# Performance work log

Measured on AMD Instinct MI355X. Metric: run time of the kernel, lower is better.

## Reference

```python
import jax, jax.numpy as jnp
import numpy as np

N_NODES = 100000
N_EDGES = 1600000
D_IN = 128
D_HID = 128
N_CLASSES = 64


def _sage_mean_layer(h, src, dst, deg, W_self, W_neigh, b):
    # gather source-node features along edges: [E, d]
    msg = h[src]
    # sum messages into destination nodes, then mean by in-degree
    agg = jax.ops.segment_sum(msg, dst, num_segments=N_NODES)
    mean_neigh = agg / deg[:, None]
    return jax.nn.relu(h @ W_self + mean_neigh @ W_neigh + b)


def setup_inputs() -> dict:
    key = jax.random.key(0)
    ks = jax.random.split(key, 9)
    s = 1.0 / np.sqrt(D_IN)
    return {
        "features": jax.random.normal(ks[0], (N_NODES, D_IN), dtype=jnp.float32),
        "src": jax.random.randint(ks[1], (N_EDGES,), 0, N_NODES, dtype=jnp.int32),
        "dst": jax.random.randint(ks[2], (N_EDGES,), 0, N_NODES, dtype=jnp.int32),
        "W_self1": jax.random.normal(ks[3], (D_IN, D_HID), dtype=jnp.float32) * s,
        "W_neigh1": jax.random.normal(ks[4], (D_IN, D_HID), dtype=jnp.float32) * s,
        "b1": jnp.zeros((D_HID,), dtype=jnp.float32),
        "W_self2": jax.random.normal(ks[5], (D_HID, D_HID), dtype=jnp.float32) * s,
        "W_neigh2": jax.random.normal(ks[6], (D_HID, D_HID), dtype=jnp.float32) * s,
        "b2": jnp.zeros((D_HID,), dtype=jnp.float32),
        "W_out": jax.random.normal(ks[7], (D_HID, N_CLASSES), dtype=jnp.float32) * s,
        "b_out": jnp.zeros((N_CLASSES,), dtype=jnp.float32),
    }


def reference(features, src, dst, W_self1, W_neigh1, b1, W_self2, W_neigh2, b2, W_out, b_out):
    # in-degree per destination node (clamped to avoid div-by-zero for isolated nodes)
    deg = jax.ops.segment_sum(jnp.ones((N_EDGES,), jnp.float32), dst, num_segments=N_NODES)
    deg = jnp.maximum(deg, 1.0)
    h = _sage_mean_layer(features, src, dst, deg, W_self1, W_neigh1, b1)
    h = _sage_mean_layer(h, src, dst, deg, W_self2, W_neigh2, b2)
    return h @ W_out + b_out  # [N_NODES, N_CLASSES] logits
```

## Files before the change

### kernel.cpp

```cpp
#include <hip/hip_runtime.h>
#include <hip/hip_bf16.h>

constexpr int N_NODES = 100000;
constexpr int N_EDGES = 1600000;
constexpr int D = 128;
constexpr int N_CLASSES = 64;

constexpr int PART_NODES = 32;
constexpr int NPART = N_NODES / PART_NODES;
constexpr int NB1 = 49;
constexpr int CAP1 = 40960;
constexpr int SUBB = 10;
constexpr int CHUNK = CAP1 / SUBB;
constexpr int CAP2 = 1024;
constexpr int NCTR2 = NB1 * 64;
constexpr int EB1 = (N_EDGES + 1023) / 1024;
constexpr int CIB = 13;
constexpr int CVTB = N_NODES * (D / 4) / 256;
constexpr int PKB = 36;

typedef __attribute__((ext_vector_type(8))) short short8;
typedef __attribute__((ext_vector_type(4))) float f32x4;
typedef __attribute__((ext_vector_type(2))) float f32x2;

static __device__ __forceinline__ float bf2f(unsigned int lo16) {
    unsigned int x = lo16 << 16;
    return __builtin_bit_cast(float, x);
}
static __device__ __forceinline__ unsigned short f2bf(float f) {
    unsigned int x = __builtin_bit_cast(unsigned int, f);
    x += 0x7fffu + ((x >> 16) & 1u);
    return (unsigned short)(x >> 16);
}
static __device__ __forceinline__ unsigned int pack4_fp8(float a, float b,
                                                         float c, float d) {
    int v = __builtin_amdgcn_cvt_pk_fp8_f32(a, b, 0, false);
    v = __builtin_amdgcn_cvt_pk_fp8_f32(c, d, v, true);
    return (unsigned int)v;
}
static __device__ __forceinline__ unsigned char f2fp8(float a) {
    return (unsigned char)(__builtin_amdgcn_cvt_pk_fp8_f32(a, a, 0, false) & 0xff);
}

__global__ __launch_bounds__(256) void prep_k(int* __restrict__ cursor1,
                                              int* __restrict__ cursor2,
                                              const float* __restrict__ feat,
                                              unsigned short* __restrict__ fbuf,
                                              unsigned int* __restrict__ f8buf,
                                              const float* __restrict__ Ws1,
                                              const float* __restrict__ Wn1,
                                              const float* __restrict__ Ws2,
                                              const float* __restrict__ Wn2,
                                              const float* __restrict__ Wo,
                                              unsigned short* __restrict__ wp1,
                                              unsigned short* __restrict__ wp2,
                                              unsigned short* __restrict__ wpo) {
    const int b = blockIdx.x;
    const int t = threadIdx.x;
    if (b < CIB) {
        int i = b * 256 + t;
        if (i < NB1) cursor1[i] = i * CAP1;
        if (i < NCTR2) cursor2[i] = i << 10;
    } else if (b < CIB + CVTB) {
        int i = (b - CIB) * 256 + t;
        float4 v = ((const float4*)feat)[i];
        ushort4 r;
        r.x = f2bf(v.x); r.y = f2bf(v.y); r.z = f2bf(v.z); r.w = f2bf(v.w);
        ((ushort4*)fbuf)[i] = r;
        f8buf[i] = pack4_fp8(v.x, v.y, v.z, v.w);
    } else {
        int g = (b - CIB - CVTB) * 4 + (t >> 6);
        if (g >= 144) return;
        int lane = t & 63;
        const float *Wa, *Wb;
        unsigned short* wp;
        int DOUT, bb;
        if (g < 64)       { Wa = Ws1; Wb = Wn1; wp = wp1; DOUT = 128; bb = g; }
        else if (g < 128) { Wa = Ws2; Wb = Wn2; wp = wp2; DOUT = 128; bb = g - 64; }
        else              { Wa = Wo;  Wb = nullptr; wp = wpo; DOUT = 64; bb = g - 128; }
        int NCT = DOUT / 16;
        int kstep = bb / NCT;
        int ct = bb % NCT;
        int col = ct * 16 + (lane & 15);
        int kbase = kstep * 32 + (lane >> 4) * 8;
        unsigned short r[8];
        #pragma unroll
        for (int j = 0; j < 8; ++j) {
            int k = kbase + j;
            float w = (k < 128) ? Wa[(size_t)k * DOUT + col]
                                : Wb[(size_t)(k - 128) * DOUT + col];
            r[j] = f2bf(w);
        }
        *(short8*)(wp + ((size_t)((kstep * NCT + ct) * 64 + lane)) * 8) =
            *(const short8*)r;
    }
}

__global__ __launch_bounds__(256) void bin1_k(const int* __restrict__ src,
                                              const int* __restrict__ dst,
                                              int* __restrict__ cursor1,
                                              unsigned int* __restrict__ pack1) {
    __shared__ unsigned int lpay[1024];
    __shared__ unsigned char lcb[1024];
    __shared__ int hist[NB1], loff[NB1], gpos[NB1], lcur[NB1];

    const int t = threadIdx.x;
    const int ebase = blockIdx.x * 1024;
    int nblk = N_EDGES - ebase;
    if (nblk > 1024) nblk = 1024;
    const bool ok = (t * 4 < nblk);

    if (t < NB1) hist[t] = 0;
    __syncthreads();

    int4 d4, s4;
    if (ok) {
        d4 = *(const int4*)(dst + ebase + t * 4);
        s4 = *(const int4*)(src + ebase + t * 4);
        atomicAdd(&hist[d4.x >> 11], 1);
        atomicAdd(&hist[d4.y >> 11], 1);
        atomicAdd(&hist[d4.z >> 11], 1);
        atomicAdd(&hist[d4.w >> 11], 1);
    }
    __syncthreads();

    if (t == 0) {
        int run = 0;
        #pragma unroll
        for (int b = 0; b < NB1; ++b) { loff[b] = run; run += hist[b]; }
    }
    __syncthreads();
    if (t < NB1) {
        gpos[t] = atomicAdd(cursor1 + t, hist[t]);
        lcur[t] = loff[t];
    }
    __syncthreads();

    if (ok) {
        #pragma unroll
        for (int k = 0; k < 4; ++k) {
            int dd = (k == 0) ? d4.x : (k == 1) ? d4.y : (k == 2) ? d4.z : d4.w;
            int ss = (k == 0) ? s4.x : (k == 1) ? s4.y : (k == 2) ? s4.z : s4.w;
            int cb = dd >> 11;
            int pos = atomicAdd(&lcur[cb], 1);
            lpay[pos] = ((unsigned int)(dd & 2047) << 17) | (unsigned int)ss;
            lcb[pos] = (unsigned char)cb;
        }
    }
    __syncthreads();

    for (int i = t; i < nblk; i += 256) {
        int cb = lcb[i];
        int op = gpos[cb] + (i - loff[cb]);
        if (op < (cb + 1) * CAP1) pack1[op] = lpay[i];
    }
}

__global__ __launch_bounds__(256) void bin2_k(const int* __restrict__ cursor1,
                                              int* __restrict__ cursor2,
                                              const unsigned int* __restrict__ pack1,
                                              unsigned int* __restrict__ pack2) {
    __shared__ unsigned int lpay[CHUNK];
    __shared__ unsigned int lsort[CHUNK];
    __shared__ int hist[64], loff[64], gpos[64], lcur[64];

    const int t = threadIdx.x;
    const int cb = blockIdx.x / SUBB;
    const int sb = blockIdx.x % SUBB;

    int cnt = cursor1[cb] - cb * CAP1;
    if (cnt > CAP1) cnt = CAP1;
    const int base = sb * CHUNK;
    int n = cnt - base;
    if (n <= 0) return;
    if (n > CHUNK) n = CHUNK;

    if (t < 64) hist[t] = 0;
    __syncthreads();

    const unsigned int* gsrc = pack1 + (size_t)cb * CAP1 + base;
    for (int i = t; i < n; i += 256) {
        unsigned int pk = gsrc[i];
        lpay[i] = pk;
        atomicAdd(&hist[pk >> 22], 1);
    }
    __syncthreads();

    if (t == 0) {
        int run = 0;
        #pragma unroll
        for (int b = 0; b < 64; ++b) { loff[b] = run; run += hist[b]; }
    }
    __syncthreads();
    if (t < 64) {
        gpos[t] = atomicAdd(cursor2 + cb * 64 + t, hist[t]);
        lcur[t] = loff[t];
    }
    __syncthreads();

    for (int i = t; i < n; i += 256) {
        unsigned int pk = lpay[i];
        int pos = atomicAdd(&lcur[pk >> 22], 1);
        lsort[pos] = pk;
    }
    __syncthreads();

    for (int i = t; i < n; i += 256) {
        unsigned int pk = lsort[i];
        int pw = pk >> 22;
        int p = cb * 64 + pw;
        int op = gpos[pw] + (i - loff[pw]);
        if (op < ((p + 1) << 10)) pack2[op] = pk & 0x003fffffu;
    }
}

template <bool OUTPROJ>
__global__ __launch_bounds__(256) void fused_k(const unsigned short* __restrict__ xin,
                                               const unsigned char* __restrict__ x8,
                                               const unsigned int* __restrict__ pack,
                                               const int* __restrict__ cursor2,
                                               const short8* __restrict__ wp,
                                               const float* __restrict__ bias,
                                               unsigned short* __restrict__ xout,
                                               unsigned char* __restrict__ x8out,
                                               const short8* __restrict__ wpo,
                                               const float* __restrict__ bout,
                                               float* __restrict__ outp) {
    __shared__ unsigned int eraw[CAP2];
    __shared__ unsigned int ssrc[CAP2];
    __shared__ int nsh;
    __shared__ int bcnt[32];
    __shared__ int boff[33];
    __shared__ unsigned short mlds[PART_NODES][136];

    const int t = threadIdx.x;
    const int p = blockIdx.x;

    if (t == 0) {
        int c = cursor2[p] - (p << 10);
        nsh = (c < CAP2) ? c : CAP2;
    }
    if (t < 32) bcnt[t] = 0;
    __syncthreads();
    const int n = nsh;

    const unsigned int* gsrc = pack + ((size_t)p << 10);
    for (int i = t; i < n; i += 256) {
        unsigned int pk = gsrc[i];
        eraw[i] = pk;
        atomicAdd(&bcnt[pk >> 17], 1);
    }
    __syncthreads();

    if (t == 0) {
        int s = 0;
        #pragma unroll
        for (int i = 0; i < 32; ++i) { boff[i] = s; s += bcnt[i]; }
        boff[32] = s;
    }
    __syncthreads();
    if (t < 32) bcnt[t] = boff[t];
    __syncthreads();

    for (int i = t; i < n; i += 256) {
        unsigned int pk = eraw[i];
        int pos = atomicAdd(&bcnt[pk >> 17], 1);
        ssrc[pos] = pk & 0x1ffffu;
    }
    __syncthreads();

    const int w = t >> 6, lane = t & 63;
    const int sub = lane >> 4;
    const int cl = lane & 15;

    for (int g = 0; g < 8; ++g) {
        const int ni = w * 8 + g;
        const int b = boff[ni];
        const int eN = boff[ni + 1];

        float acc[8];
        #pragma unroll
        for (int r = 0; r < 8; ++r) acc[r] = 0.f;

        int i = b + sub;
        for (; i + 4 < eN; i += 8) {
            int s0 = ssrc[i];
            int s1 = ssrc[i + 4];
            uint2 u0 = *(const uint2*)(x8 + (size_t)s0 * 128 + cl * 8);
            uint2 u1 = *(const uint2*)(x8 + (size_t)s1 * 128 + cl * 8);
            f32x2 q;
            q = __builtin_amdgcn_cvt_pk_f32_fp8(u0.x, false); acc[0] += q[0]; acc[1] += q[1];
            q = __builtin_amdgcn_cvt_pk_f32_fp8(u0.x, true);  acc[2] += q[0]; acc[3] += q[1];
            q = __builtin_amdgcn_cvt_pk_f32_fp8(u0.y, false); acc[4] += q[0]; acc[5] += q[1];
            q = __builtin_amdgcn_cvt_pk_f32_fp8(u0.y, true);  acc[6] += q[0]; acc[7] += q[1];
            q = __builtin_amdgcn_cvt_pk_f32_fp8(u1.x, false); acc[0] += q[0]; acc[1] += q[1];
            q = __builtin_amdgcn_cvt_pk_f32_fp8(u1.x, true);  acc[2] += q[0]; acc[3] += q[1];
            q = __builtin_amdgcn_cvt_pk_f32_fp8(u1.y, false); acc[4] += q[0]; acc[5] += q[1];
            q = __builtin_amdgcn_cvt_pk_f32_fp8(u1.y, true);  acc[6] += q[0]; acc[7] += q[1];
        }
        if (i < eN) {
            int s0 = ssrc[i];
            uint2 u0 = *(const uint2*)(x8 + (size_t)s0 * 128 + cl * 8);
            f32x2 q;
            q = __builtin_amdgcn_cvt_pk_f32_fp8(u0.x, false); acc[0] += q[0]; acc[1] += q[1];
            q = __builtin_amdgcn_cvt_pk_f32_fp8(u0.x, true);  acc[2] += q[0]; acc[3] += q[1];
            q = __builtin_amdgcn_cvt_pk_f32_fp8(u0.y, false); acc[4] += q[0]; acc[5] += q[1];
            q = __builtin_amdgcn_cvt_pk_f32_fp8(u0.y, true);  acc[6] += q[0]; acc[7] += q[1];
        }
        #pragma unroll
        for (int r = 0; r < 8; ++r) {
            acc[r] += __shfl_xor(acc[r], 16);
            acc[r] += __shfl_xor(acc[r], 32);
        }
        float inv = 1.0f / fmaxf((float)(eN - b), 1.0f);
        float lo = acc[sub * 2 + 0] * inv;
        float hi = acc[sub * 2 + 1] * inv;
        unsigned int o = ((unsigned int)f2bf(hi) << 16) | (unsigned int)f2bf(lo);
        *(unsigned int*)(&mlds[ni][cl * 8 + sub * 2]) = o;
    }
    __syncthreads();

    const int frag = w & 1;
    const int cg0 = (w >> 1) * 4;
    const int r15 = lane & 15;
    const int khi = lane >> 4;
    const int row0 = p * PART_NODES + frag * 16;
    const unsigned short* arow = xin + (size_t)(row0 + r15) * 128 + khi * 8;

    f32x4 acc[4];
    #pragma unroll
    for (int c = 0; c < 4; ++c) acc[c] = {0.f, 0.f, 0.f, 0.f};

    #pragma unroll
    for (int ks = 0; ks < 8; ++ks) {
        short8 a;
        if (ks < 4) a = *(const short8*)(arow + ks * 32);
        else        a = *(const short8*)(&mlds[frag * 16 + r15][(ks - 4) * 32 + khi * 8]);
        #pragma unroll
        for (int c = 0; c < 4; ++c) {
            short8 b = wp[(ks * 8 + cg0 + c) * 64 + lane];
            acc[c] = __builtin_amdgcn_mfma_f32_16x16x32_bf16(a, b, acc[c], 0, 0, 0);
        }
    }

    const int rhi = khi, col0 = r15;
    if (!OUTPROJ) {
        #pragma unroll
        for (int c = 0; c < 4; ++c) {
            float bv = bias[(cg0 + c) * 16 + col0];
            #pragma unroll
            for (int j = 0; j < 4; ++j) {
                float v = fmaxf(acc[c][j] + bv, 0.f);
                size_t off = (size_t)(row0 + rhi * 4 + j) * 128 + (cg0 + c) * 16 + col0;
                xout[off] = f2bf(v);
                x8out[off] = f2fp8(v);
            }
        }
    } else {
        __syncthreads();
        #pragma unroll
        for (int c = 0; c < 4; ++c) {
            float bv = bias[(cg0 + c) * 16 + col0];
            #pragma unroll
            for (int j = 0; j < 4; ++j) {
                float v = fmaxf(acc[c][j] + bv, 0.f);
                mlds[frag * 16 + rhi * 4 + j][(cg0 + c) * 16 + col0] = f2bf(v);
            }
        }
        __syncthreads();
        const int frag2 = w & 1;
        const int ct0 = (w >> 1) * 2;
        f32x4 oacc[2];
        oacc[0] = {0.f, 0.f, 0.f, 0.f};
        oacc[1] = {0.f, 0.f, 0.f, 0.f};
        #pragma unroll
        for (int ks = 0; ks < 4; ++ks) {
            short8 a = *(const short8*)(&mlds[frag2 * 16 + r15][ks * 32 + khi * 8]);
            #pragma unroll
            for (int c = 0; c < 2; ++c) {
                short8 b = wpo[(ks * 4 + ct0 + c) * 64 + lane];
                oacc[c] = __builtin_amdgcn_mfma_f32_16x16x32_bf16(a, b, oacc[c], 0, 0, 0);
            }
        }
        #pragma unroll
        for (int c = 0; c < 2; ++c) {
            float bv = bout[(ct0 + c) * 16 + col0];
            #pragma unroll
            for (int j = 0; j < 4; ++j) {
                outp[(size_t)(p * PART_NODES + frag2 * 16 + rhi * 4 + j) * N_CLASSES
                     + (ct0 + c) * 16 + col0] = oacc[c][j] + bv;
            }
        }
    }
}

extern "C" void kernel_launch(void* const* d_in, const int* in_sizes, int n_in,
                              void* d_out, int out_size, void* d_ws, size_t ws_size,
                              hipStream_t stream) {
    const float* feat   = (const float*)d_in[0];
    const int*   src    = (const int*)d_in[1];
    const int*   dst    = (const int*)d_in[2];
    const float* Wself1 = (const float*)d_in[3];
    const float* Wneigh1= (const float*)d_in[4];
    const float* b1     = (const float*)d_in[5];
    const float* Wself2 = (const float*)d_in[6];
    const float* Wneigh2= (const float*)d_in[7];
    const float* b2     = (const float*)d_in[8];
    const float* Wout   = (const float*)d_in[9];
    const float* bout   = (const float*)d_in[10];
    float* out = (float*)d_out;
    (void)ws_size;

    int* cursor1 = (int*)d_ws;
    int* cursor2 = cursor1 + 64;
    unsigned int* pack1 = (unsigned int*)(cursor2 + NCTR2);
    unsigned int* pack2 = pack1 + (size_t)NB1 * CAP1;
    unsigned short* fbuf1 = (unsigned short*)(pack2 + (size_t)NCTR2 * CAP2);
    unsigned short* h1    = fbuf1 + (size_t)N_NODES * D;
    unsigned int* f8feat  = (unsigned int*)(h1 + (size_t)N_NODES * D);
    unsigned int* h1f8    = f8feat + (size_t)N_NODES * (D / 4);
    unsigned short* wp1   = (unsigned short*)(h1f8 + (size_t)N_NODES * (D / 4));
    unsigned short* wp2   = wp1 + 256 * 128;
    unsigned short* wpo   = wp2 + 256 * 128;

    prep_k<<<CIB + CVTB + PKB, 256, 0, stream>>>(cursor1, cursor2, feat,
                                                 fbuf1, f8feat,
                                                 Wself1, Wneigh1, Wself2, Wneigh2,
                                                 Wout, wp1, wp2, wpo);

    bin1_k<<<EB1, 256, 0, stream>>>(src, dst, cursor1, pack1);
    bin2_k<<<NB1 * SUBB, 256, 0, stream>>>(cursor1, cursor2, pack1, pack2);

    fused_k<false><<<NPART, 256, 0, stream>>>(fbuf1, (const unsigned char*)f8feat,
                                              pack2, cursor2,
                                              (const short8*)wp1, b1, h1,
                                              (unsigned char*)h1f8,
                                              nullptr, nullptr, nullptr);

    fused_k<true><<<NPART, 256, 0, stream>>>(h1, (const unsigned char*)h1f8,
                                             pack2, cursor2,
                                             (const short8*)wp2, b2, nullptr, nullptr,
                                             (const short8*)wpo, bout, out);
}
```

Measured before the change: 177.9 us.

## Merge edge binning into prep kernel, memset cursors, unroll gather by four

```diff
diff --git a/kernel.cpp b/kernel.cpp
--- a/kernel.cpp
+++ b/kernel.cpp
@@ -15,7 +15,6 @@
 constexpr int CAP2 = 1024;
 constexpr int NCTR2 = NB1 * 64;
 constexpr int EB1 = (N_EDGES + 1023) / 1024;
-constexpr int CIB = 13;
 constexpr int CVTB = N_NODES * (D / 4) / 256;
 constexpr int PKB = 36;
 
@@ -41,9 +40,18 @@
 static __device__ __forceinline__ unsigned char f2fp8(float a) {
     return (unsigned char)(__builtin_amdgcn_cvt_pk_fp8_f32(a, a, 0, false) & 0xff);
 }
-
-__global__ __launch_bounds__(256) void prep_k(int* __restrict__ cursor1,
-                                              int* __restrict__ cursor2,
+static __device__ __forceinline__ void dec8(uint2 u, float* acc) {
+    f32x2 q;
+    q = __builtin_amdgcn_cvt_pk_f32_fp8(u.x, false); acc[0] += q[0]; acc[1] += q[1];
+    q = __builtin_amdgcn_cvt_pk_f32_fp8(u.x, true);  acc[2] += q[0]; acc[3] += q[1];
+    q = __builtin_amdgcn_cvt_pk_f32_fp8(u.y, false); acc[4] += q[0]; acc[5] += q[1];
+    q = __builtin_amdgcn_cvt_pk_f32_fp8(u.y, true);  acc[6] += q[0]; acc[7] += q[1];
+}
+
+__global__ __launch_bounds__(256) void prep_k(const int* __restrict__ src,
+                                              const int* __restrict__ dst,
+                                              int* __restrict__ cursor1,
+                                              unsigned int* __restrict__ pack1,
                                               const float* __restrict__ feat,
                                               unsigned short* __restrict__ fbuf,
                                               unsigned int* __restrict__ f8buf,
@@ -55,21 +63,72 @@
                                               unsigned short* __restrict__ wp1,
                                               unsigned short* __restrict__ wp2,
                                               unsigned short* __restrict__ wpo) {
+    __shared__ unsigned int lpay[1024];
+    __shared__ unsigned char lcb[1024];
+    __shared__ int hist[NB1], loff[NB1], gpos[NB1], lcur[NB1];
+
     const int b = blockIdx.x;
     const int t = threadIdx.x;
-    if (b < CIB) {
-        int i = b * 256 + t;
-        if (i < NB1) cursor1[i] = i * CAP1;
-        if (i < NCTR2) cursor2[i] = i << 10;
-    } else if (b < CIB + CVTB) {
-        int i = (b - CIB) * 256 + t;
+
+    if (b < EB1) {
+        const int ebase = b * 1024;
+        int nblk = N_EDGES - ebase;
+        if (nblk > 1024) nblk = 1024;
+        const bool ok = (t * 4 < nblk);
+
+        if (t < NB1) hist[t] = 0;
+        __syncthreads();
+
+        int4 d4, s4;
+        if (ok) {
+            d4 = *(const int4*)(dst + ebase + t * 4);
+            s4 = *(const int4*)(src + ebase + t * 4);
+            atomicAdd(&hist[d4.x >> 11], 1);
+            atomicAdd(&hist[d4.y >> 11], 1);
+            atomicAdd(&hist[d4.z >> 11], 1);
+            atomicAdd(&hist[d4.w >> 11], 1);
+        }
+        __syncthreads();
+
+        if (t == 0) {
+            int run = 0;
+            #pragma unroll
+            for (int k = 0; k < NB1; ++k) { loff[k] = run; run += hist[k]; }
+        }
+        __syncthreads();
+        if (t < NB1) {
+            gpos[t] = atomicAdd(cursor1 + t, hist[t]);
+            lcur[t] = loff[t];
+        }
+        __syncthreads();
+
+        if (ok) {
+            #pragma unroll
+            for (int k = 0; k < 4; ++k) {
+                int dd = (k == 0) ? d4.x : (k == 1) ? d4.y : (k == 2) ? d4.z : d4.w;
+                int ss = (k == 0) ? s4.x : (k == 1) ? s4.y : (k == 2) ? s4.z : s4.w;
+                int cb = dd >> 11;
+                int pos = atomicAdd(&lcur[cb], 1);
+                lpay[pos] = ((unsigned int)(dd & 2047) << 17) | (unsigned int)ss;
+                lcb[pos] = (unsigned char)cb;
+            }
+        }
+        __syncthreads();
+
+        for (int i = t; i < nblk; i += 256) {
+            int cb = lcb[i];
+            int rel = gpos[cb] + (i - loff[cb]);
+            if (rel < CAP1) pack1[(size_t)cb * CAP1 + rel] = lpay[i];
+        }
+    } else if (b < EB1 + CVTB) {
+        int i = (b - EB1) * 256 + t;
         float4 v = ((const float4*)feat)[i];
         ushort4 r;
         r.x = f2bf(v.x); r.y = f2bf(v.y); r.z = f2bf(v.z); r.w = f2bf(v.w);
         ((ushort4*)fbuf)[i] = r;
         f8buf[i] = pack4_fp8(v.x, v.y, v.z, v.w);
     } else {
-        int g = (b - CIB - CVTB) * 4 + (t >> 6);
+        int g = (b - EB1 - CVTB) * 4 + (t >> 6);
         if (g >= 144) return;
         int lane = t & 63;
         const float *Wa, *Wb;
@@ -96,66 +155,6 @@
     }
 }
 
-__global__ __launch_bounds__(256) void bin1_k(const int* __restrict__ src,
-                                              const int* __restrict__ dst,
-                                              int* __restrict__ cursor1,
-                                              unsigned int* __restrict__ pack1) {
-    __shared__ unsigned int lpay[1024];
-    __shared__ unsigned char lcb[1024];
-    __shared__ int hist[NB1], loff[NB1], gpos[NB1], lcur[NB1];
-
-    const int t = threadIdx.x;
-    const int ebase = blockIdx.x * 1024;
-    int nblk = N_EDGES - ebase;
-    if (nblk > 1024) nblk = 1024;
-    const bool ok = (t * 4 < nblk);
-
-    if (t < NB1) hist[t] = 0;
-    __syncthreads();
-
-    int4 d4, s4;
-    if (ok) {
-        d4 = *(const int4*)(dst + ebase + t * 4);
-        s4 = *(const int4*)(src + ebase + t * 4);
-        atomicAdd(&hist[d4.x >> 11], 1);
-        atomicAdd(&hist[d4.y >> 11], 1);
-        atomicAdd(&hist[d4.z >> 11], 1);
-        atomicAdd(&hist[d4.w >> 11], 1);
-    }
-    __syncthreads();
-
-    if (t == 0) {
-        int run = 0;
-        #pragma unroll
-        for (int b = 0; b < NB1; ++b) { loff[b] = run; run += hist[b]; }
-    }
-    __syncthreads();
-    if (t < NB1) {
-        gpos[t] = atomicAdd(cursor1 + t, hist[t]);
-        lcur[t] = loff[t];
-    }
-    __syncthreads();
-
-    if (ok) {
-        #pragma unroll
-        for (int k = 0; k < 4; ++k) {
-            int dd = (k == 0) ? d4.x : (k == 1) ? d4.y : (k == 2) ? d4.z : d4.w;
-            int ss = (k == 0) ? s4.x : (k == 1) ? s4.y : (k == 2) ? s4.z : s4.w;
-            int cb = dd >> 11;
-            int pos = atomicAdd(&lcur[cb], 1);
-            lpay[pos] = ((unsigned int)(dd & 2047) << 17) | (unsigned int)ss;
-            lcb[pos] = (unsigned char)cb;
-        }
-    }
-    __syncthreads();
-
-    for (int i = t; i < nblk; i += 256) {
-        int cb = lcb[i];
-        int op = gpos[cb] + (i - loff[cb]);
-        if (op < (cb + 1) * CAP1) pack1[op] = lpay[i];
-    }
-}
-
 __global__ __launch_bounds__(256) void bin2_k(const int* __restrict__ cursor1,
                                               int* __restrict__ cursor2,
                                               const unsigned int* __restrict__ pack1,
@@ -168,7 +167,7 @@
     const int cb = blockIdx.x / SUBB;
     const int sb = blockIdx.x % SUBB;
 
-    int cnt = cursor1[cb] - cb * CAP1;
+    int cnt = cursor1[cb];
     if (cnt > CAP1) cnt = CAP1;
     const int base = sb * CHUNK;
     int n = cnt - base;
@@ -189,7 +188,7 @@
     if (t == 0) {
         int run = 0;
         #pragma unroll
-        for (int b = 0; b < 64; ++b) { loff[b] = run; run += hist[b]; }
+        for (int k = 0; k < 64; ++k) { loff[k] = run; run += hist[k]; }
     }
     __syncthreads();
     if (t < 64) {
@@ -209,8 +208,8 @@
         unsigned int pk = lsort[i];
         int pw = pk >> 22;
         int p = cb * 64 + pw;
-        int op = gpos[pw] + (i - loff[pw]);
-        if (op < ((p + 1) << 10)) pack2[op] = pk & 0x003fffffu;
+        int rel = gpos[pw] + (i - loff[pw]);
+        if (rel < CAP2) pack2[((size_t)p << 10) + rel] = pk & 0x003fffffu;
     }
 }
 
@@ -237,7 +236,7 @@
     const int p = blockIdx.x;
 
     if (t == 0) {
-        int c = cursor2[p] - (p << 10);
+        int c = cursor2[p];
         nsh = (c < CAP2) ? c : CAP2;
     }
     if (t < 32) bcnt[t] = 0;
@@ -271,6 +270,7 @@
 
     const int w = t >> 6, lane = t & 63;
     const int sub = lane >> 4;
+    const int cl8 = (lane & 15) * 8;
     const int cl = lane & 15;
 
     for (int g = 0; g < 8; ++g) {
@@ -283,29 +283,24 @@
         for (int r = 0; r < 8; ++r) acc[r] = 0.f;
 
         int i = b + sub;
+        for (; i + 12 < eN; i += 16) {
+            unsigned s0 = ssrc[i], s1 = ssrc[i + 4], s2 = ssrc[i + 8], s3 = ssrc[i + 12];
+            uint2 u0 = *(const uint2*)(x8 + ((s0 << 7) + cl8));
+            uint2 u1 = *(const uint2*)(x8 + ((s1 << 7) + cl8));
+            uint2 u2 = *(const uint2*)(x8 + ((s2 << 7) + cl8));
+            uint2 u3 = *(const uint2*)(x8 + ((s3 << 7) + cl8));
+            dec8(u0, acc); dec8(u1, acc); dec8(u2, acc); dec8(u3, acc);
+        }
         for (; i + 4 < eN; i += 8) {
-            int s0 = ssrc[i];
-            int s1 = ssrc[i + 4];
-            uint2 u0 = *(const uint2*)(x8 + (size_t)s0 * 128 + cl * 8);
-            uint2 u1 = *(const uint2*)(x8 + (size_t)s1 * 128 + cl * 8);
-            f32x2 q;
-            q = __builtin_amdgcn_cvt_pk_f32_fp8(u0.x, false); acc[0] += q[0]; acc[1] += q[1];
-            q = __builtin_amdgcn_cvt_pk_f32_fp8(u0.x, true);  acc[2] += q[0]; acc[3] += q[1];
-            q = __builtin_amdgcn_cvt_pk_f32_fp8(u0.y, false); acc[4] += q[0]; acc[5] += q[1];
-            q = __builtin_amdgcn_cvt_pk_f32_fp8(u0.y, true);  acc[6] += q[0]; acc[7] += q[1];
-            q = __builtin_amdgcn_cvt_pk_f32_fp8(u1.x, false); acc[0] += q[0]; acc[1] += q[1];
-            q = __builtin_amdgcn_cvt_pk_f32_fp8(u1.x, true);  acc[2] += q[0]; acc[3] += q[1];
-            q = __builtin_amdgcn_cvt_pk_f32_fp8(u1.y, false); acc[4] += q[0]; acc[5] += q[1];
-            q = __builtin_amdgcn_cvt_pk_f32_fp8(u1.y, true);  acc[6] += q[0]; acc[7] += q[1];
+            unsigned s0 = ssrc[i], s1 = ssrc[i + 4];
+            uint2 u0 = *(const uint2*)(x8 + ((s0 << 7) + cl8));
+            uint2 u1 = *(const uint2*)(x8 + ((s1 << 7) + cl8));
+            dec8(u0, acc); dec8(u1, acc);
         }
         if (i < eN) {
-            int s0 = ssrc[i];
-            uint2 u0 = *(const uint2*)(x8 + (size_t)s0 * 128 + cl * 8);
-            f32x2 q;
-            q = __builtin_amdgcn_cvt_pk_f32_fp8(u0.x, false); acc[0] += q[0]; acc[1] += q[1];
-            q = __builtin_amdgcn_cvt_pk_f32_fp8(u0.x, true);  acc[2] += q[0]; acc[3] += q[1];
-            q = __builtin_amdgcn_cvt_pk_f32_fp8(u0.y, false); acc[4] += q[0]; acc[5] += q[1];
-            q = __builtin_amdgcn_cvt_pk_f32_fp8(u0.y, true);  acc[6] += q[0]; acc[7] += q[1];
+            unsigned s0 = ssrc[i];
+            uint2 u0 = *(const uint2*)(x8 + ((s0 << 7) + cl8));
+            dec8(u0, acc);
         }
         #pragma unroll
         for (int r = 0; r < 8; ++r) {
@@ -423,12 +418,13 @@
     unsigned short* wp2   = wp1 + 256 * 128;
     unsigned short* wpo   = wp2 + 256 * 128;
 
-    prep_k<<<CIB + CVTB + PKB, 256, 0, stream>>>(cursor1, cursor2, feat,
-                                                 fbuf1, f8feat,
+    hipMemsetAsync(cursor1, 0, (64 + NCTR2) * sizeof(int), stream);
+
+    prep_k<<<EB1 + CVTB + PKB, 256, 0, stream>>>(src, dst, cursor1, pack1,
+                                                 feat, fbuf1, f8feat,
                                                  Wself1, Wneigh1, Wself2, Wneigh2,
                                                  Wout, wp1, wp2, wpo);
 
-    bin1_k<<<EB1, 256, 0, stream>>>(src, dst, cursor1, pack1);
     bin2_k<<<NB1 * SUBB, 256, 0, stream>>>(cursor1, cursor2, pack1, pack2);
 
     fused_k<false><<<NPART, 256, 0, stream>>>(fbuf1, (const unsigned char*)f8feat,
```

New measurement: 190.7 us. 1.07x slower.
